# Performance work log

Hardware: AMD Instinct MI355X
Metric: run time of the kernel (lower is better)

Reference implementation:

```python
import jax, jax.numpy as jnp
import numpy as np

B, V, C = 4, 50000, 160


def rotation_6d_to_matrix(d6):
    """pytorch3d-style 6D rotation -> 3x3 matrix (rows b1,b2,b3)."""
    a1, a2 = d6[..., :3], d6[..., 3:]
    eps = 1e-8
    b1 = a1 / jnp.maximum(jnp.linalg.norm(a1, axis=-1, keepdims=True), eps)
    a2p = a2 - jnp.sum(b1 * a2, axis=-1, keepdims=True) * b1
    b2 = a2p / jnp.maximum(jnp.linalg.norm(a2p, axis=-1, keepdims=True), eps)
    b3 = jnp.cross(b1, b2)
    return jnp.stack([b1, b2, b3], axis=-2)  # (..., 3, 3)


def setup_inputs() -> dict:
    key = jax.random.key(0)
    k1, k2, k3, k4, k5 = jax.random.split(key, 5)
    X = jax.random.normal(k1, (B, V, 3), dtype=jnp.float32)
    V_nodes = jax.random.normal(k2, (B, C, 3), dtype=jnp.float32) * 0.1
    rot6d_nodes = jax.random.normal(k3, (B, C, 6), dtype=jnp.float32)
    W_nodes = jax.random.uniform(k4, (V, C), dtype=jnp.float32)
    W_nodes = W_nodes / jnp.sum(W_nodes, axis=1, keepdims=True)  # row-normalized skinning weights
    idx_nn_to_nodes = jax.random.randint(k5, (C,), 0, V, dtype=jnp.int64)
    return {"X": X, "V_nodes": V_nodes, "rot6d_nodes": rot6d_nodes,
            "W_nodes": W_nodes, "idx_nn_to_nodes": idx_nn_to_nodes}


def reference(X, V_nodes, rot6d_nodes, W_nodes, idx_nn_to_nodes):
    # R: (B, C, 3, 3)
    R = rotation_6d_to_matrix(rot6d_nodes)
    # gather node centers: (B, C, 3)
    center = X[:, idx_nn_to_nodes, :]
    # disp: (B, V, C, 3)
    disp = X[:, :, None, :] - center[:, None, :, :]
    # rotate displacement by per-node rotation, add back center + node offset
    Rdisp = jnp.einsum('bvcd,bckd->bvck', disp, R) \
            + center[:, None, :, :] + V_nodes[:, None, :, :]  # (B, V, C, 3)
    # weighted skinning sum over nodes: (B, V, 3)
    out = jnp.einsum('vc,bvck->bvk', W_nodes, Rdisp)
    return out
```

## Files before the change

kernel.cpp:

```cpp
#include <hip/hip_runtime.h>

#define Bv 4
#define Vv 50000
#define Cv 160
#define TILES 782
#define WSTR 168

typedef unsigned short u16;
typedef unsigned int   u32;
typedef __attribute__((ext_vector_type(8))) short bf16x8;
typedef __attribute__((ext_vector_type(4))) float f32x4;

__device__ __forceinline__ u16 f2bf(float f) {
    u32 u = __float_as_uint(f);
    return (u16)((u + 0x7FFFu + ((u >> 16) & 1u)) >> 16);
}

__global__ void precompute_AT(const float* __restrict__ X,
                              const float* __restrict__ Vn,
                              const float* __restrict__ r6,
                              const int* __restrict__ idx,
                              u16* __restrict__ AT) {
    int i = blockIdx.x * blockDim.x + threadIdx.x;
    if (i >= Bv * Cv) return;
    int b = i / Cv, c = i % Cv;

    const float* d6 = r6 + (size_t)(b * Cv + c) * 6;
    float a1x = d6[0], a1y = d6[1], a1z = d6[2];
    float a2x = d6[3], a2y = d6[4], a2z = d6[5];

    float n1 = fmaxf(sqrtf(a1x*a1x + a1y*a1y + a1z*a1z), 1e-8f);
    float b1x = a1x / n1, b1y = a1y / n1, b1z = a1z / n1;

    float d = b1x*a2x + b1y*a2y + b1z*a2z;
    float px = a2x - d*b1x, py = a2y - d*b1y, pz = a2z - d*b1z;
    float n2 = fmaxf(sqrtf(px*px + py*py + pz*pz), 1e-8f);
    float b2x = px / n2, b2y = py / n2, b2z = pz / n2;

    float b3x = b1y*b2z - b1z*b2y;
    float b3y = b1z*b2x - b1x*b2z;
    float b3z = b1x*b2y - b1y*b2x;

    int iv = idx[c];
    const float* xc = X + ((size_t)b * Vv + iv) * 3;
    float cx = xc[0], cy = xc[1], cz = xc[2];
    const float* vn = Vn + (size_t)(b * Cv + c) * 3;
    float vx = vn[0], vy = vn[1], vz = vn[2];

    float vals[12];
    vals[0] = b1x; vals[1]  = b1y; vals[2]  = b1z;
    vals[3] = b2x; vals[4]  = b2y; vals[5]  = b2z;
    vals[6] = b3x; vals[7]  = b3y; vals[8]  = b3z;
    vals[9]  = cx + vx - (b1x*cx + b1y*cy + b1z*cz);
    vals[10] = cy + vy - (b2x*cx + b2y*cy + b2z*cz);
    vals[11] = cz + vz - (b3x*cx + b3y*cy + b3z*cz);

#pragma unroll
    for (int j = 0; j < 12; ++j)
        AT[(size_t)(b * 12 + j) * Cv + c] = f2bf(vals[j]);
}

__global__ __launch_bounds__(256) void deform_mfma(const float* __restrict__ X,
                                                   const float* __restrict__ W,
                                                   const u16* __restrict__ ATg,
                                                   float* __restrict__ out) {
    __shared__ char smem[64 * WSTR * 2];
    u16*   Wl = (u16*)smem;
    float* P  = (float*)smem;

    const int tid = threadIdx.x;
    const int v0  = blockIdx.x * 64;

    for (int i = tid; i < 64 * 40; i += 256) {
        int r = i / 40, c4 = i % 40;
        int row = v0 + r;
        if (row >= Vv) row = Vv - 1;
        float4 q = ((const float4*)(W + (size_t)row * Cv))[c4];
        ushort4 h;
        h.x = f2bf(q.x); h.y = f2bf(q.y); h.z = f2bf(q.z); h.w = f2bf(q.w);
        *(ushort4*)&Wl[r * WSTR + c4 * 4] = h;
    }
    __syncthreads();

    const int lane = tid & 63;
    const int wv   = tid >> 6;
    const int m    = lane & 15;
    const int quad = lane >> 4;

    bf16x8 afr[5];
#pragma unroll
    for (int kt = 0; kt < 5; ++kt)
        afr[kt] = *(const bf16x8*)&Wl[(wv * 16 + m) * WSTR + kt * 32 + quad * 8];

    bf16x8 bfr[3][5];
#pragma unroll
    for (int nt = 0; nt < 3; ++nt)
#pragma unroll
        for (int kt = 0; kt < 5; ++kt)
            bfr[nt][kt] = *(const bf16x8*)&ATg[(size_t)(nt * 16 + m) * Cv + kt * 32 + quad * 8];

    f32x4 acc[3] = {{0,0,0,0},{0,0,0,0},{0,0,0,0}};
#pragma unroll
    for (int kt = 0; kt < 5; ++kt)
#pragma unroll
        for (int nt = 0; nt < 3; ++nt)
            acc[nt] = __builtin_amdgcn_mfma_f32_16x16x32_bf16(afr[kt], bfr[nt][kt], acc[nt], 0, 0, 0);

    __syncthreads();

#pragma unroll
    for (int nt = 0; nt < 3; ++nt)
#pragma unroll
        for (int r = 0; r < 4; ++r)
            P[(wv * 16 + quad * 4 + r) * 49 + nt * 16 + m] = acc[nt][r];
    __syncthreads();

    const int b  = tid >> 6;
    const int vl = tid & 63;
    const int v  = v0 + vl;
    if (v < Vv) {
        const float* p = &P[vl * 49 + b * 12];
        const float* xp = X + ((size_t)b * Vv + v) * 3;
        float x0 = xp[0], x1 = xp[1], x2 = xp[2];
        float* op = out + ((size_t)b * Vv + v) * 3;
        op[0] = p[0]*x0 + p[1]*x1 + p[2]*x2 + p[9];
        op[1] = p[3]*x0 + p[4]*x1 + p[5]*x2 + p[10];
        op[2] = p[6]*x0 + p[7]*x1 + p[8]*x2 + p[11];
    }
}

extern "C" void kernel_launch(void* const* d_in, const int* in_sizes, int n_in,
                              void* d_out, int out_size, void* d_ws, size_t ws_size,
                              hipStream_t stream) {
    const float* X   = (const float*)d_in[0];
    const float* Vn  = (const float*)d_in[1];
    const float* r6  = (const float*)d_in[2];
    const float* W   = (const float*)d_in[3];
    const int*   idx = (const int*)d_in[4];
    float* out = (float*)d_out;

    u16* AT = (u16*)d_ws;

    precompute_AT<<<(Bv * Cv + 255) / 256, 256, 0, stream>>>(X, Vn, r6, idx, AT);
    deform_mfma<<<TILES, 256, 0, stream>>>(X, W, AT, out);
}
```

Baseline: 87.99 us.

## Fuse node transform precompute into main MFMA kernel via shared memory

Removes the separate precompute kernel and has every block recompute the per-node rotation/offset matrix directly into LDS, then feed MFMA B-fragments from LDS. W tile loads are issued into registers before the recompute to overlap global latency. This eliminates a launch and the global workspace round-trip but duplicates the node computation in every block and increases LDS usage, which may reduce occupancy.

```diff
diff --git a/kernel.cpp b/kernel.cpp
--- a/kernel.cpp
+++ b/kernel.cpp
@@ -16,68 +16,74 @@
     return (u16)((u + 0x7FFFu + ((u >> 16) & 1u)) >> 16);
 }
 
-__global__ void precompute_AT(const float* __restrict__ X,
-                              const float* __restrict__ Vn,
-                              const float* __restrict__ r6,
-                              const int* __restrict__ idx,
-                              u16* __restrict__ AT) {
-    int i = blockIdx.x * blockDim.x + threadIdx.x;
-    if (i >= Bv * Cv) return;
-    int b = i / Cv, c = i % Cv;
-
-    const float* d6 = r6 + (size_t)(b * Cv + c) * 6;
-    float a1x = d6[0], a1y = d6[1], a1z = d6[2];
-    float a2x = d6[3], a2y = d6[4], a2z = d6[5];
-
-    float n1 = fmaxf(sqrtf(a1x*a1x + a1y*a1y + a1z*a1z), 1e-8f);
-    float b1x = a1x / n1, b1y = a1y / n1, b1z = a1z / n1;
-
-    float d = b1x*a2x + b1y*a2y + b1z*a2z;
-    float px = a2x - d*b1x, py = a2y - d*b1y, pz = a2z - d*b1z;
-    float n2 = fmaxf(sqrtf(px*px + py*py + pz*pz), 1e-8f);
-    float b2x = px / n2, b2y = py / n2, b2z = pz / n2;
-
-    float b3x = b1y*b2z - b1z*b2y;
-    float b3y = b1z*b2x - b1x*b2z;
-    float b3z = b1x*b2y - b1y*b2x;
-
-    int iv = idx[c];
-    const float* xc = X + ((size_t)b * Vv + iv) * 3;
-    float cx = xc[0], cy = xc[1], cz = xc[2];
-    const float* vn = Vn + (size_t)(b * Cv + c) * 3;
-    float vx = vn[0], vy = vn[1], vz = vn[2];
-
-    float vals[12];
-    vals[0] = b1x; vals[1]  = b1y; vals[2]  = b1z;
-    vals[3] = b2x; vals[4]  = b2y; vals[5]  = b2z;
-    vals[6] = b3x; vals[7]  = b3y; vals[8]  = b3z;
-    vals[9]  = cx + vx - (b1x*cx + b1y*cy + b1z*cz);
-    vals[10] = cy + vy - (b2x*cx + b2y*cy + b2z*cz);
-    vals[11] = cz + vz - (b3x*cx + b3y*cy + b3z*cz);
-
-#pragma unroll
-    for (int j = 0; j < 12; ++j)
-        AT[(size_t)(b * 12 + j) * Cv + c] = f2bf(vals[j]);
-}
-
-__global__ __launch_bounds__(256) void deform_mfma(const float* __restrict__ X,
-                                                   const float* __restrict__ W,
-                                                   const u16* __restrict__ ATg,
-                                                   float* __restrict__ out) {
-    __shared__ char smem[64 * WSTR * 2];
-    u16*   Wl = (u16*)smem;
-    float* P  = (float*)smem;
+__global__ __launch_bounds__(256) void deform_fused(const float* __restrict__ X,
+                                                    const float* __restrict__ Vn,
+                                                    const float* __restrict__ r6,
+                                                    const int* __restrict__ idx,
+                                                    const float* __restrict__ W,
+                                                    float* __restrict__ out) {
+    __shared__ u16   Wl[64 * WSTR];
+    __shared__ u16   ATl[48 * WSTR];
+    __shared__ float P[64 * 49];
 
     const int tid = threadIdx.x;
     const int v0  = blockIdx.x * 64;
 
-    for (int i = tid; i < 64 * 40; i += 256) {
-        int r = i / 40, c4 = i % 40;
+    float4 wq[10];
+#pragma unroll
+    for (int t = 0; t < 10; ++t) {
+        int i  = tid + t * 256;
+        int r  = i / 40, c4 = i % 40;
         int row = v0 + r;
         if (row >= Vv) row = Vv - 1;
-        float4 q = ((const float4*)(W + (size_t)row * Cv))[c4];
+        wq[t] = ((const float4*)(W + (size_t)row * Cv))[c4];
+    }
+
+    for (int i = tid; i < Bv * Cv; i += 256) {
+        int b = i / Cv, c = i % Cv;
+
+        const float* d6 = r6 + (size_t)(b * Cv + c) * 6;
+        float a1x = d6[0], a1y = d6[1], a1z = d6[2];
+        float a2x = d6[3], a2y = d6[4], a2z = d6[5];
+
+        float n1 = fmaxf(sqrtf(a1x*a1x + a1y*a1y + a1z*a1z), 1e-8f);
+        float b1x = a1x / n1, b1y = a1y / n1, b1z = a1z / n1;
+
+        float d = b1x*a2x + b1y*a2y + b1z*a2z;
+        float px = a2x - d*b1x, py = a2y - d*b1y, pz = a2z - d*b1z;
+        float n2 = fmaxf(sqrtf(px*px + py*py + pz*pz), 1e-8f);
+        float b2x = px / n2, b2y = py / n2, b2z = pz / n2;
+
+        float b3x = b1y*b2z - b1z*b2y;
+        float b3y = b1z*b2x - b1x*b2z;
+        float b3z = b1x*b2y - b1y*b2x;
+
+        int iv = idx[c];
+        const float* xc = X + ((size_t)b * Vv + iv) * 3;
+        float cx = xc[0], cy = xc[1], cz = xc[2];
+        const float* vn = Vn + (size_t)(b * Cv + c) * 3;
+        float vx = vn[0], vy = vn[1], vz = vn[2];
+
+        float vals[12];
+        vals[0] = b1x; vals[1]  = b1y; vals[2]  = b1z;
+        vals[3] = b2x; vals[4]  = b2y; vals[5]  = b2z;
+        vals[6] = b3x; vals[7]  = b3y; vals[8]  = b3z;
+        vals[9]  = cx + vx - (b1x*cx + b1y*cy + b1z*cz);
+        vals[10] = cy + vy - (b2x*cx + b2y*cy + b2z*cz);
+        vals[11] = cz + vz - (b3x*cx + b3y*cy + b3z*cz);
+
+#pragma unroll
+        for (int j = 0; j < 12; ++j)
+            ATl[(b * 12 + j) * WSTR + c] = f2bf(vals[j]);
+    }
+
+#pragma unroll
+    for (int t = 0; t < 10; ++t) {
+        int i  = tid + t * 256;
+        int r  = i / 40, c4 = i % 40;
         ushort4 h;
-        h.x = f2bf(q.x); h.y = f2bf(q.y); h.z = f2bf(q.z); h.w = f2bf(q.w);
+        h.x = f2bf(wq[t].x); h.y = f2bf(wq[t].y);
+        h.z = f2bf(wq[t].z); h.w = f2bf(wq[t].w);
         *(ushort4*)&Wl[r * WSTR + c4 * 4] = h;
     }
     __syncthreads();
@@ -97,7 +103,7 @@
     for (int nt = 0; nt < 3; ++nt)
 #pragma unroll
         for (int kt = 0; kt < 5; ++kt)
-            bfr[nt][kt] = *(const bf16x8*)&ATg[(size_t)(nt * 16 + m) * Cv + kt * 32 + quad * 8];
+            bfr[nt][kt] = *(const bf16x8*)&ATl[(nt * 16 + m) * WSTR + kt * 32 + quad * 8];
 
     f32x4 acc[3] = {{0,0,0,0},{0,0,0,0},{0,0,0,0}};
 #pragma unroll
@@ -105,8 +111,6 @@
 #pragma unroll
         for (int nt = 0; nt < 3; ++nt)
             acc[nt] = __builtin_amdgcn_mfma_f32_16x16x32_bf16(afr[kt], bfr[nt][kt], acc[nt], 0, 0, 0);
-
-    __syncthreads();
 
 #pragma unroll
     for (int nt = 0; nt < 3; ++nt)
@@ -119,7 +123,7 @@
     const int vl = tid & 63;
     const int v  = v0 + vl;
     if (v < Vv) {
-        const float* p = &P[vl * 49 + b * 12];
+        const float* p  = &P[vl * 49 + b * 12];
         const float* xp = X + ((size_t)b * Vv + v) * 3;
         float x0 = xp[0], x1 = xp[1], x2 = xp[2];
         float* op = out + ((size_t)b * Vv + v) * 3;
@@ -139,8 +143,5 @@
     const int*   idx = (const int*)d_in[4];
     float* out = (float*)d_out;
 
-    u16* AT = (u16*)d_ws;
-
-    precompute_AT<<<(Bv * Cv + 255) / 256, 256, 0, stream>>>(X, Vn, r6, idx, AT);
-    deform_mfma<<<TILES, 256, 0, stream>>>(X, W, AT, out);
+    deform_fused<<<TILES, 256, 0, stream>>>(X, Vn, r6, idx, W, out);
 }
```

Result: no change. 89.00 us (+1.1%).
